# Performance work log

Hardware: AMD Instinct MI355X
Metric: run time of the kernel (lower is better)

The kernel has to match this reference:

```python
import jax, jax.numpy as jnp
import numpy as np

NEG_INF = -1e30


def setup_inputs() -> dict:
    B, S, H, N, T = 128, 512, 512, 256, 40960
    key = jax.random.key(0)
    ks = jax.random.split(key, 20)
    sc = 1.0 / np.sqrt(H)
    inp = {
        'tok_feat': jax.random.normal(ks[0], (B, S, H), jnp.float32),
        'ast_h': jax.random.normal(ks[1], (T, H), jnp.float32),
        'cfg_feat': jax.random.normal(ks[2], (B, N, H), jnp.float32),
        'W_tok': jax.random.normal(ks[3], (H, H), jnp.float32) * sc,
        'b_tok': jax.random.normal(ks[4], (H,), jnp.float32) * 0.01,
        'v_tok': jax.random.normal(ks[5], (H,), jnp.float32) * sc,
        'c_tok': jnp.float32(0.0),
        'W_ast': jax.random.normal(ks[6], (H, H), jnp.float32) * sc,
        'b_ast': jax.random.normal(ks[7], (H,), jnp.float32) * 0.01,
        'v_ast': jax.random.normal(ks[8], (H,), jnp.float32) * sc,
        'c_ast': jnp.float32(0.0),
        'W_cfg': jax.random.normal(ks[9], (H, H), jnp.float32) * sc,
        'b_cfg': jax.random.normal(ks[10], (H,), jnp.float32) * 0.01,
        'v_cfg': jax.random.normal(ks[11], (H,), jnp.float32) * sc,
        'c_cfg': jnp.float32(0.0),
        'W_fuse': jax.random.normal(ks[12], (3 * H, H), jnp.float32) * (1.0 / np.sqrt(3 * H)),
        'b_fuse': jax.random.normal(ks[13], (H,), jnp.float32) * 0.01,
        'tok_len': jax.random.randint(ks[14], (B,), 1, S + 1, jnp.int64),
        # ragged AST: sorted segment ids covering T nodes, here equal-size segments
        'node_seg': jnp.repeat(jnp.arange(B, dtype=jnp.int32), T // B),
        'cfg_node_mask': jax.random.randint(ks[15], (B, N), 0, 2, jnp.int32).at[:, 0].set(1),
    }
    return inp


def reference(tok_feat, ast_h, cfg_feat,
              W_tok, b_tok, v_tok, c_tok,
              W_ast, b_ast, v_ast, c_ast,
              W_cfg, b_cfg, v_cfg, c_cfg,
              W_fuse, b_fuse,
              tok_len, node_seg, cfg_node_mask):
    B, S, H = tok_feat.shape
    N = cfg_feat.shape[1]

    # ---- Token modality: masked softmax attention pooling ----
    tok_logit = jnp.tanh(tok_feat @ W_tok + b_tok) @ v_tok + c_tok          # [B,S]
    tok_mask = jnp.arange(S)[None, :] < tok_len[:, None]                    # [B,S]
    tok_w = jax.nn.softmax(jnp.where(tok_mask, tok_logit, NEG_INF), axis=1)
    tok_pool = jnp.einsum('bs,bsh->bh', tok_w, tok_feat)                    # [B,H]

    # ---- AST modality: ragged segment softmax attention pooling ----
    ast_logit = jnp.tanh(ast_h @ W_ast + b_ast) @ v_ast + c_ast             # [T]
    seg_max = jax.ops.segment_max(ast_logit, node_seg, num_segments=B)
    e = jnp.exp(ast_logit - seg_max[node_seg])
    denom = jax.ops.segment_sum(e, node_seg, num_segments=B)
    ast_w = e / denom[node_seg]                                             # [T]
    ast_pool = jax.ops.segment_sum(ast_w[:, None] * ast_h, node_seg, num_segments=B)  # [B,H]

    # ---- CFG modality: masked sigmoid-gated pooling ----
    cfg_logit = jnp.tanh(cfg_feat @ W_cfg + b_cfg) @ v_cfg + c_cfg          # [B,N]
    gate = jax.nn.sigmoid(cfg_logit) * cfg_node_mask.astype(cfg_feat.dtype)
    cfg_pool = jnp.einsum('bn,bnh->bh', gate, cfg_feat)                     # [B,H]

    # ---- Modal fusion ----
    concat = jnp.concatenate([tok_pool, ast_pool, cfg_pool], axis=1)        # [B,3H]
    code_feat = jnp.tanh(concat @ W_fuse + b_fuse)                          # [B,H]
    return code_feat
```

## Files before the change

### kernel.cpp

```cpp
#include <hip/hip_runtime.h>
#include <stdint.h>

#define HD 512

typedef __bf16 bf16x8 __attribute__((ext_vector_type(8)));
typedef __bf16 bf16x4 __attribute__((ext_vector_type(4)));
typedef float  f32x4  __attribute__((ext_vector_type(4)));

union BF8U { uint4 u; bf16x8 v; };

__device__ __forceinline__ float fast_tanh(float x) {
  x = fminf(15.f, fmaxf(-15.f, x));
  float e = __expf(2.f * x);
  return (e - 1.f) * __builtin_amdgcn_rcpf(e + 1.f);
}
__device__ __forceinline__ float fast_sigmoid(float x) {
  return __builtin_amdgcn_rcpf(1.f + __expf(-x));
}

__global__ void setup_kernel(const float* __restrict__ W0, const float* __restrict__ W1,
                             const float* __restrict__ W2, unsigned short* __restrict__ WbAll,
                             float4* __restrict__ zdst, int nz,
                             const int* __restrict__ seg, int* __restrict__ ss,
                             int* __restrict__ se, int T) {
  int blk = blockIdx.x, t = threadIdx.x;
  if (blk < 192) {
    int mat = blk >> 6, chunk = blk & 63;
    const float* W = (mat == 0) ? W0 : ((mat == 1) ? W1 : W2);
    int np = chunk >> 4, kt = chunk & 15;
    int jl = t & 127, kh = t >> 7;
    int j = np * 128 + jl;
    int nt = jl >> 4;
    unsigned short* base = WbAll + (size_t)mat * 262144 + (size_t)chunk * 4096 + nt * 512;
#pragma unroll
    for (int i = 0; i < 16; ++i) {
      int kk = kh * 16 + i;
      float v = W[(size_t)(kt * 32 + kk) * HD + j];
      int l = (kk >> 3) * 16 + (jl & 15);
      int jj = kk & 7;
      union { __bf16 h; unsigned short u; } cv;
      cv.h = (__bf16)v;
      base[l * 8 + jj] = cv.u;
    }
  } else if (blk < 384) {
    int i = (blk - 192) * 256 + t;
    if (i < nz) zdst[i] = make_float4(0.f, 0.f, 0.f, 0.f);
  } else {
    int tt = (blk - 384) * 256 + t;
    if (tt < T) {
      int s = seg[tt];
      if (tt == 0 || seg[tt - 1] != s) ss[s] = tt;
      if (tt == T - 1 || seg[tt + 1] != s) se[s] = tt + 1;
    }
  }
}

__global__ __launch_bounds__(512, 4) void gemm_all_kernel(
    const float* __restrict__ A0, const float* __restrict__ A1, const float* __restrict__ A2,
    const unsigned short* __restrict__ WbAll,
    const float* __restrict__ b0, const float* __restrict__ v0,
    const float* __restrict__ b1, const float* __restrict__ v1,
    const float* __restrict__ b2, const float* __restrict__ v2,
    const int* __restrict__ tokLen, int nTok, int nAst,
    float* __restrict__ lg0, float* __restrict__ lg1, float* __restrict__ lg2)
{
  int bm = blockIdx.x;
  const float* A; const unsigned short* Wb; const float* bias; const float* vvec;
  float* logit; int lb;
  if (bm < nTok) {
    lb = bm; A = A0; Wb = WbAll; bias = b0; vvec = v0; logit = lg0;
    bool i64 = (tokLen[1] == 0);
    int b = lb >> 3;
    int len = i64 ? tokLen[2 * b] : tokLen[b];
    if (((lb & 7) * 64) >= len) return;
  } else if (bm < nTok + nAst) {
    lb = bm - nTok; A = A1; Wb = WbAll + 262144; bias = b1; vvec = v1; logit = lg1;
  } else {
    lb = bm - nTok - nAst; A = A2; Wb = WbAll + 524288; bias = b2; vvec = v2; logit = lg2;
  }
  size_t m0 = (size_t)lb * 64;

  int tid = threadIdx.x, wave = tid >> 6, lane = tid & 63;
  int wn = wave;

  __shared__ __align__(16) char AshB[2][4096];
  __shared__ float redS[8][64];

  const float* aSrc = A + (m0 + (tid >> 3)) * HD + (tid & 7) * 4;
  const int rowS = tid >> 3, qS = tid & 7;
  const int srW = rowS >> 1;
  const int wA = srW * 128 + 16 * ((((rowS & 1) << 2) + (qS >> 1)) ^ (srW & 7)) + (qS & 1) * 8;

  const char* srcB = (const char*)Wb + (size_t)(wn >> 1) * 131072 +
                     (wn & 1) * 4096 + lane * 16;

  const int aRd = ((lane & 15) >> 1) * 128 +
                  16 * ((4 * (lane & 1) + (lane >> 4)) ^ ((lane & 15) >> 1));

  float4 a4;
  auto loadA = [&](float4& dst, int kt) {
    dst = *(const float4*)(aSrc + kt * 32);
  };
  auto writeA = [&](int buf, const float4& ar) {
    bf16x4 w0;
    w0[0] = (__bf16)ar.x; w0[1] = (__bf16)ar.y; w0[2] = (__bf16)ar.z; w0[3] = (__bf16)ar.w;
    *(bf16x4*)(&AshB[buf][0] + wA) = w0;
  };
  auto loadB = [&](bf16x8 (&dst)[4], int kt) {
    const char* sB = srcB + (size_t)kt * 8192;
#pragma unroll
    for (int ntl = 0; ntl < 4; ++ntl) {
      BF8U bu;
      bu.u = *(const uint4*)(sB + ntl * 1024);
      dst[ntl] = bu.v;
    }
  };

  f32x4 acc[4][4];
#pragma unroll
  for (int i = 0; i < 4; ++i)
#pragma unroll
    for (int j = 0; j < 4; ++j) acc[i][j] = (f32x4){0.f, 0.f, 0.f, 0.f};

  bf16x8 bfA[4], bfB[4];

  {
    float4 t4;
    loadA(t4, 0);
    writeA(0, t4);
    loadA(a4, 1);
    loadB(bfA, 0);
    asm volatile("s_waitcnt lgkmcnt(0)" ::: "memory");
    __builtin_amdgcn_s_barrier();
  }

  auto body = [&](int kt, bf16x8 (&cur)[4], bf16x8 (&nxt)[4]) {
    if (kt < 15) loadB(nxt, kt + 1);
    const char* aBuf = &AshB[kt & 1][0];
    {
      bf16x8 af2[2];
      af2[0] = *(const bf16x8*)(aBuf + 0 * 1024 + aRd);
      af2[1] = *(const bf16x8*)(aBuf + 1 * 1024 + aRd);
#pragma unroll
      for (int mt = 0; mt < 2; ++mt)
#pragma unroll
        for (int ntl = 0; ntl < 4; ++ntl)
          acc[mt][ntl] = __builtin_amdgcn_mfma_f32_16x16x32_bf16(af2[mt], cur[ntl], acc[mt][ntl], 0, 0, 0);
    }
    {
      bf16x8 af2[2];
      af2[0] = *(const bf16x8*)(aBuf + 2 * 1024 + aRd);
      af2[1] = *(const bf16x8*)(aBuf + 3 * 1024 + aRd);
#pragma unroll
      for (int mt = 0; mt < 2; ++mt)
#pragma unroll
        for (int ntl = 0; ntl < 4; ++ntl)
          acc[2 + mt][ntl] = __builtin_amdgcn_mfma_f32_16x16x32_bf16(af2[mt], cur[ntl], acc[2 + mt][ntl], 0, 0, 0);
    }
    if (kt < 15) {
      writeA((kt + 1) & 1, a4);
      if (kt < 14) loadA(a4, kt + 2);
      asm volatile("s_waitcnt lgkmcnt(0)" ::: "memory");
      __builtin_amdgcn_s_barrier();
    }
  };

#pragma unroll
  for (int kt = 0; kt < 16; kt += 2) {
    body(kt, bfA, bfB);
    body(kt + 1, bfB, bfA);
  }

  float part[4][4];
#pragma unroll
  for (int mt = 0; mt < 4; ++mt)
#pragma unroll
    for (int i = 0; i < 4; ++i) part[mt][i] = 0.f;

  const int colBase = wn * 64;
#pragma unroll
  for (int ntl = 0; ntl < 4; ++ntl) {
    int j = colBase + ntl * 16 + (lane & 15);
    float bj = bias[j], vj = vvec[j];
#pragma unroll
    for (int mt = 0; mt < 4; ++mt)
#pragma unroll
      for (int i = 0; i < 4; ++i)
        part[mt][i] += fast_tanh(acc[mt][ntl][i] + bj) * vj;
  }
#pragma unroll
  for (int off = 8; off >= 1; off >>= 1)
#pragma unroll
    for (int mt = 0; mt < 4; ++mt)
#pragma unroll
      for (int i = 0; i < 4; ++i)
        part[mt][i] += __shfl_xor(part[mt][i], off, 64);

  if ((lane & 15) == 0) {
    int rloc = (lane >> 4) * 4;
#pragma unroll
    for (int mt = 0; mt < 4; ++mt)
#pragma unroll
      for (int i = 0; i < 4; ++i)
        redS[wn][mt * 16 + rloc + i] = part[mt][i];
  }
  __syncthreads();
  if (tid < 64) {
    float s = 0.f;
#pragma unroll
    for (int w = 0; w < 8; ++w) s += redS[w][tid];
    logit[m0 + tid] = s;
  }
}

__global__ void pool_all_kernel(
    const float* __restrict__ tokf, const float* __restrict__ lgT, const int* __restrict__ tl,
    const float* __restrict__ astf, const float* __restrict__ lgA,
    const int* __restrict__ ss, const int* __restrict__ se,
    const float* __restrict__ cfgf, const float* __restrict__ lgC,
    const int* __restrict__ mask, const float* __restrict__ cptr,
    float* __restrict__ pools)
{
  int b = blockIdx.x, chz = blockIdx.y, tid = threadIdx.x;
  __shared__ float redm[4], reds[4];
  __shared__ float wsh[128];
  int wv = tid >> 6, ln = tid & 63;

  if (chz < 4) {
    int ch = chz;
    bool i64 = (tl[1] == 0);
    int len = i64 ? tl[2 * b] : tl[b];
    if (ch * 128 >= len) return;
    const float* lg = lgT + b * 512;
    float x0 = (tid < len) ? lg[tid] : -1e30f;
    float x1 = (tid + 256 < len) ? lg[tid + 256] : -1e30f;
    float m = fmaxf(x0, x1);
#pragma unroll
    for (int off = 32; off; off >>= 1) m = fmaxf(m, __shfl_xor(m, off, 64));
    if (ln == 0) redm[wv] = m;
    __syncthreads();
    float bm = fmaxf(fmaxf(redm[0], redm[1]), fmaxf(redm[2], redm[3]));
    float s = ((tid < len) ? __expf(x0 - bm) : 0.f) + ((tid + 256 < len) ? __expf(x1 - bm) : 0.f);
#pragma unroll
    for (int off = 32; off; off >>= 1) s += __shfl_xor(s, off, 64);
    if (ln == 0) reds[wv] = s;
    __syncthreads();
    float bs = reds[0] + reds[1] + reds[2] + reds[3];
    float rb = __builtin_amdgcn_rcpf(bs);
    if (tid < 128) {
      int sidx = ch * 128 + tid;
      wsh[tid] = (sidx < len) ? __expf(lg[sidx] - bm) * rb : 0.f;
    }
    __syncthreads();
    int cnt = min(128, len - ch * 128);
    int h = tid * 2;
    float2 acc = make_float2(0.f, 0.f);
    const float* fb = tokf + ((size_t)b * 512 + ch * 128) * HD + h;
#pragma unroll 4
    for (int s2 = 0; s2 < cnt; ++s2) {
      float2 f = *(const float2*)(fb + (size_t)s2 * HD);
      acc.x += wsh[s2] * f.x; acc.y += wsh[s2] * f.y;
    }
    atomicAdd(&pools[b * 512 + h], acc.x);
    atomicAdd(&pools[b * 512 + h + 1], acc.y);
  } else if (chz < 8) {
    int ch = chz - 4;
    int t0 = ss[b], t1 = se[b];
    int len = t1 - t0;
    if (len <= 0) return;
    float m = -1e30f;
    for (int t = t0 + tid; t < t1; t += 256) m = fmaxf(m, lgA[t]);
#pragma unroll
    for (int off = 32; off; off >>= 1) m = fmaxf(m, __shfl_xor(m, off, 64));
    if (ln == 0) redm[wv] = m;
    __syncthreads();
    float bm = fmaxf(fmaxf(redm[0], redm[1]), fmaxf(redm[2], redm[3]));
    float s = 0.f;
    for (int t = t0 + tid; t < t1; t += 256) s += __expf(lgA[t] - bm);
#pragma unroll
    for (int off = 32; off; off >>= 1) s += __shfl_xor(s, off, 64);
    if (ln == 0) reds[wv] = s;
    __syncthreads();
    float bs = reds[0] + reds[1] + reds[2] + reds[3];
    float r = __builtin_amdgcn_rcpf(bs);
    int per = (len + 3) >> 2;
    int a0 = t0 + ch * per;
    int a1 = min(t1, a0 + per);
    int h = tid * 2;
    float2 acc = make_float2(0.f, 0.f);
    for (int base = a0; base < a1; base += 128) {
      int cnt = min(128, a1 - base);
      __syncthreads();
      if (tid < cnt) wsh[tid] = __expf(lgA[base + tid] - bm) * r;
      __syncthreads();
      for (int s2 = 0; s2 < cnt; ++s2) {
        float2 f = *(const float2*)(astf + (size_t)(base + s2) * HD + h);
        acc.x += wsh[s2] * f.x; acc.y += wsh[s2] * f.y;
      }
    }
    atomicAdd(&pools[65536 + b * 512 + h], acc.x);
    atomicAdd(&pools[65536 + b * 512 + h + 1], acc.y);
  } else {
    int ch = chz - 8;
    float cc = cptr[0];
    int n0 = ch * 128;
    if (tid < 128) {
      int n = n0 + tid;
      float g = fast_sigmoid(lgC[b * 256 + n] + cc);
      wsh[tid] = mask[b * 256 + n] ? g : 0.f;
    }
    __syncthreads();
    int h = tid * 2;
    float2 acc = make_float2(0.f, 0.f);
    const float* fb = cfgf + ((size_t)b * 256 + n0) * HD + h;
#pragma unroll 4
    for (int s2 = 0; s2 < 128; ++s2) {
      float2 f = *(const float2*)(fb + (size_t)s2 * HD);
      acc.x += wsh[s2] * f.x; acc.y += wsh[s2] * f.y;
    }
    atomicAdd(&pools[131072 + b * 512 + h], acc.x);
    atomicAdd(&pools[131072 + b * 512 + h + 1], acc.y);
  }
}

__global__ void fuse_partial_kernel(const float* __restrict__ pools,
                                    const float* __restrict__ Wf,
                                    float* __restrict__ fpart) {
  int bg = blockIdx.x, kc = blockIdx.y;
  int tid = threadIdx.x;
  int bq = tid >> 7, jt = tid & 127;
  __shared__ float psh[8][128];
  for (int idx = tid; idx < 8 * 128; idx += 256) {
    int bb = idx >> 7, kk = idx & 127;
    int i = kc * 128 + kk;
    psh[bb][kk] = pools[(size_t)(i >> 9) * 65536 + (size_t)(bg * 8 + bb) * 512 + (i & 511)];
  }
  __syncthreads();
  f32x4 acc[4];
#pragma unroll
  for (int bb = 0; bb < 4; ++bb) acc[bb] = (f32x4){0.f, 0.f, 0.f, 0.f};
  const float* wrow = Wf + (size_t)(kc * 128) * 512 + jt * 4;
#pragma unroll 4
  for (int k = 0; k < 128; ++k) {
    float4 wv = *(const float4*)(wrow + (size_t)k * 512);
#pragma unroll
    for (int bb = 0; bb < 4; ++bb) {
      float p = psh[bq * 4 + bb][k];
      acc[bb][0] += p * wv.x; acc[bb][1] += p * wv.y;
      acc[bb][2] += p * wv.z; acc[bb][3] += p * wv.w;
    }
  }
  float* dst = fpart + (size_t)kc * 65536 + (size_t)(bg * 8 + bq * 4) * 512 + jt * 4;
#pragma unroll
  for (int bb = 0; bb < 4; ++bb)
    *(f32x4*)(dst + (size_t)bb * 512) = acc[bb];
}

__global__ void finalize_kernel(const float* __restrict__ fpart, const float* __restrict__ bfuse,
                                float* __restrict__ out) {
  int idx = blockIdx.x * 256 + threadIdx.x;
  float s = bfuse[idx & 511];
#pragma unroll
  for (int kc = 0; kc < 12; ++kc) s += fpart[(size_t)kc * 65536 + idx];
  out[idx] = fast_tanh(s);
}

static constexpr size_t OFF_WB_ALL = 0;
static constexpr size_t OFF_LG_TOK = 1536 * 1024;
static constexpr size_t OFF_LG_AST = OFF_LG_TOK + 65536 * 4;
static constexpr size_t OFF_LG_CFG = OFF_LG_AST + 40960 * 4;
static constexpr size_t OFF_POOLS  = OFF_LG_CFG + 32768 * 4;
static constexpr size_t OFF_SS     = OFF_POOLS + 3 * 65536 * 4;
static constexpr size_t OFF_SE     = OFF_SS + 512;
static constexpr size_t OFF_FPART  = OFF_SE + 512;
static constexpr int    ZERO_N4    = (3 * 65536 * 4) / 16;

extern "C" void kernel_launch(void* const* d_in, const int* in_sizes, int n_in,
                              void* d_out, int out_size, void* d_ws, size_t ws_size,
                              hipStream_t stream) {
  const float* tok_feat = (const float*)d_in[0];
  const float* ast_h    = (const float*)d_in[1];
  const float* cfg_feat = (const float*)d_in[2];
  const float* W_tok = (const float*)d_in[3];
  const float* b_tok = (const float*)d_in[4];
  const float* v_tok = (const float*)d_in[5];
  const float* W_ast = (const float*)d_in[7];
  const float* b_ast = (const float*)d_in[8];
  const float* v_ast = (const float*)d_in[9];
  const float* W_cfg = (const float*)d_in[11];
  const float* b_cfg = (const float*)d_in[12];
  const float* v_cfg = (const float*)d_in[13];
  const float* c_cfg = (const float*)d_in[14];
  const float* W_fuse = (const float*)d_in[15];
  const float* b_fuse = (const float*)d_in[16];
  const int* tok_len  = (const int*)d_in[17];
  const int* node_seg = (const int*)d_in[18];
  const int* cfg_mask = (const int*)d_in[19];

  const int M_tok = in_sizes[0] / HD;
  const int T_ast = in_sizes[1] / HD;
  const int M_cfg = in_sizes[2] / HD;
  const int nTok = M_tok / 64, nAst = T_ast / 64, nCfg = M_cfg / 64;

  char* ws = (char*)d_ws;
  unsigned short* wbAll = (unsigned short*)(ws + OFF_WB_ALL);
  float* lgTok = (float*)(ws + OFF_LG_TOK);
  float* lgAst = (float*)(ws + OFF_LG_AST);
  float* lgCfg = (float*)(ws + OFF_LG_CFG);
  float* pools = (float*)(ws + OFF_POOLS);
  int*   ss    = (int*)(ws + OFF_SS);
  int*   se    = (int*)(ws + OFF_SE);
  float* fpart = (float*)(ws + OFF_FPART);

  int segBlks = (T_ast + 255) / 256;
  setup_kernel<<<384 + segBlks, 256, 0, stream>>>(
      W_tok, W_ast, W_cfg, wbAll, (float4*)(ws + OFF_POOLS), ZERO_N4,
      node_seg, ss, se, T_ast);

  gemm_all_kernel<<<nTok + nAst + nCfg, 512, 0, stream>>>(
      tok_feat, ast_h, cfg_feat, wbAll,
      b_tok, v_tok, b_ast, v_ast, b_cfg, v_cfg,
      tok_len, nTok, nAst, lgTok, lgAst, lgCfg);

  pool_all_kernel<<<dim3(128, 10), 256, 0, stream>>>(
      tok_feat, lgTok, tok_len,
      ast_h, lgAst, ss, se,
      cfg_feat, lgCfg, cfg_mask, c_cfg, pools);

  fuse_partial_kernel<<<dim3(16, 12), 256, 0, stream>>>(pools, W_fuse, fpart);
  finalize_kernel<<<256, 256, 0, stream>>>(fpart, b_fuse, (float*)d_out);
}
```

Measured before the change: 158.1 us.

## Retile logit GEMM to 128-row blocks split across two column halves with atomics

Each GEMM workgroup now covers 128 rows and half of the 512 output columns, so each wave handles 32 columns across 8 M-tiles instead of 64 columns across 4. The two column halves combine their partial logits with atomicAdd, which means the logit buffers must be zeroed, so the setup kernel's zeroing range is extended to cover them. A loads are widened to 8 floats per thread. The aim is to get more reuse of each B fragment from registers and fewer B global loads per MFMA, at the cost of atomics, extra zeroing, and coarser 128-row skipping of masked token rows.

```diff
diff --git a/kernel.cpp b/kernel.cpp
--- a/kernel.cpp
+++ b/kernel.cpp
@@ -4,7 +4,6 @@
 #define HD 512
 
 typedef __bf16 bf16x8 __attribute__((ext_vector_type(8)));
-typedef __bf16 bf16x4 __attribute__((ext_vector_type(4)));
 typedef float  f32x4  __attribute__((ext_vector_type(4)));
 
 union BF8U { uint4 u; bf16x8 v; };
@@ -42,11 +41,11 @@
       cv.h = (__bf16)v;
       base[l * 8 + jj] = cv.u;
     }
-  } else if (blk < 384) {
+  } else if (blk < 576) {
     int i = (blk - 192) * 256 + t;
     if (i < nz) zdst[i] = make_float4(0.f, 0.f, 0.f, 0.f);
   } else {
-    int tt = (blk - 384) * 256 + t;
+    int tt = (blk - 576) * 256 + t;
     if (tt < T) {
       int s = seg[tt];
       if (tt == 0 || seg[tt - 1] != s) ss[s] = tt;
@@ -72,60 +71,62 @@
     bool i64 = (tokLen[1] == 0);
     int b = lb >> 3;
     int len = i64 ? tokLen[2 * b] : tokLen[b];
-    if (((lb & 7) * 64) >= len) return;
+    if ((((lb >> 1) & 3) * 128) >= len) return;
   } else if (bm < nTok + nAst) {
     lb = bm - nTok; A = A1; Wb = WbAll + 262144; bias = b1; vvec = v1; logit = lg1;
   } else {
     lb = bm - nTok - nAst; A = A2; Wb = WbAll + 524288; bias = b2; vvec = v2; logit = lg2;
   }
-  size_t m0 = (size_t)lb * 64;
+  int r = lb >> 1, c = lb & 1;
+  size_t m0 = (size_t)r * 128;
 
   int tid = threadIdx.x, wave = tid >> 6, lane = tid & 63;
   int wn = wave;
 
-  __shared__ __align__(16) char AshB[2][4096];
-  __shared__ float redS[8][64];
-
-  const float* aSrc = A + (m0 + (tid >> 3)) * HD + (tid & 7) * 4;
-  const int rowS = tid >> 3, qS = tid & 7;
+  __shared__ __align__(16) char AshB[2][8192];
+  __shared__ float redS[8][128];
+
+  const float* aSrc = A + (m0 + (tid >> 2)) * HD + (tid & 3) * 8;
+  const int rowS = tid >> 2, qS = tid & 3;
   const int srW = rowS >> 1;
-  const int wA = srW * 128 + 16 * ((((rowS & 1) << 2) + (qS >> 1)) ^ (srW & 7)) + (qS & 1) * 8;
-
-  const char* srcB = (const char*)Wb + (size_t)(wn >> 1) * 131072 +
-                     (wn & 1) * 4096 + lane * 16;
+  const int wA = srW * 128 + 16 * ((((rowS & 1) << 2) + qS) ^ (srW & 7));
+
+  const char* srcB = (const char*)Wb + (size_t)(c * 2 + (wn >> 2)) * 131072 +
+                     ((wn & 3) * 2) * 1024 + lane * 16;
 
   const int aRd = ((lane & 15) >> 1) * 128 +
                   16 * ((4 * (lane & 1) + (lane >> 4)) ^ ((lane & 15) >> 1));
 
-  float4 a4;
-  auto loadA = [&](float4& dst, int kt) {
-    dst = *(const float4*)(aSrc + kt * 32);
+  float4 a4[2];
+  auto loadA = [&](float4 (&dst)[2], int kt) {
+    const float* p = aSrc + kt * 32;
+    dst[0] = *(const float4*)(p);
+    dst[1] = *(const float4*)(p + 4);
   };
-  auto writeA = [&](int buf, const float4& ar) {
-    bf16x4 w0;
-    w0[0] = (__bf16)ar.x; w0[1] = (__bf16)ar.y; w0[2] = (__bf16)ar.z; w0[3] = (__bf16)ar.w;
-    *(bf16x4*)(&AshB[buf][0] + wA) = w0;
+  auto writeA = [&](int buf, const float4 (&ar)[2]) {
+    bf16x8 w0;
+    w0[0] = (__bf16)ar[0].x; w0[1] = (__bf16)ar[0].y; w0[2] = (__bf16)ar[0].z; w0[3] = (__bf16)ar[0].w;
+    w0[4] = (__bf16)ar[1].x; w0[5] = (__bf16)ar[1].y; w0[6] = (__bf16)ar[1].z; w0[7] = (__bf16)ar[1].w;
+    *(bf16x8*)(&AshB[buf][0] + wA) = w0;
   };
-  auto loadB = [&](bf16x8 (&dst)[4], int kt) {
+  auto loadB = [&](bf16x8 (&dst)[2], int kt) {
     const char* sB = srcB + (size_t)kt * 8192;
-#pragma unroll
-    for (int ntl = 0; ntl < 4; ++ntl) {
-      BF8U bu;
-      bu.u = *(const uint4*)(sB + ntl * 1024);
-      dst[ntl] = bu.v;
-    }
+    BF8U bu0, bu1;
+    bu0.u = *(const uint4*)(sB);
+    bu1.u = *(const uint4*)(sB + 1024);
+    dst[0] = bu0.v; dst[1] = bu1.v;
   };
 
-  f32x4 acc[4][4];
-#pragma unroll
-  for (int i = 0; i < 4; ++i)
-#pragma unroll
-    for (int j = 0; j < 4; ++j) acc[i][j] = (f32x4){0.f, 0.f, 0.f, 0.f};
-
-  bf16x8 bfA[4], bfB[4];
+  f32x4 acc[8][2];
+#pragma unroll
+  for (int i = 0; i < 8; ++i)
+#pragma unroll
+    for (int j = 0; j < 2; ++j) acc[i][j] = (f32x4){0.f, 0.f, 0.f, 0.f};
+
+  bf16x8 bfA[2], bfB[2];
 
   {
-    float4 t4;
+    float4 t4[2];
     loadA(t4, 0);
     writeA(0, t4);
     loadA(a4, 1);
@@ -134,28 +135,20 @@
     __builtin_amdgcn_s_barrier();
   }
 
-  auto body = [&](int kt, bf16x8 (&cur)[4], bf16x8 (&nxt)[4]) {
+  auto body = [&](int kt, bf16x8 (&cur)[2], bf16x8 (&nxt)[2]) {
     if (kt < 15) loadB(nxt, kt + 1);
     const char* aBuf = &AshB[kt & 1][0];
-    {
+#pragma unroll
+    for (int mg = 0; mg < 4; ++mg) {
       bf16x8 af2[2];
-      af2[0] = *(const bf16x8*)(aBuf + 0 * 1024 + aRd);
-      af2[1] = *(const bf16x8*)(aBuf + 1 * 1024 + aRd);
-#pragma unroll
-      for (int mt = 0; mt < 2; ++mt)
-#pragma unroll
-        for (int ntl = 0; ntl < 4; ++ntl)
-          acc[mt][ntl] = __builtin_amdgcn_mfma_f32_16x16x32_bf16(af2[mt], cur[ntl], acc[mt][ntl], 0, 0, 0);
-    }
-    {
-      bf16x8 af2[2];
-      af2[0] = *(const bf16x8*)(aBuf + 2 * 1024 + aRd);
-      af2[1] = *(const bf16x8*)(aBuf + 3 * 1024 + aRd);
-#pragma unroll
-      for (int mt = 0; mt < 2; ++mt)
-#pragma unroll
-        for (int ntl = 0; ntl < 4; ++ntl)
-          acc[2 + mt][ntl] = __builtin_amdgcn_mfma_f32_16x16x32_bf16(af2[mt], cur[ntl], acc[2 + mt][ntl], 0, 0, 0);
+      af2[0] = *(const bf16x8*)(aBuf + (mg * 2 + 0) * 1024 + aRd);
+      af2[1] = *(const bf16x8*)(aBuf + (mg * 2 + 1) * 1024 + aRd);
+#pragma unroll
+      for (int m2 = 0; m2 < 2; ++m2)
+#pragma unroll
+        for (int ntl = 0; ntl < 2; ++ntl)
+          acc[mg * 2 + m2][ntl] =
+              __builtin_amdgcn_mfma_f32_16x16x32_bf16(af2[m2], cur[ntl], acc[mg * 2 + m2][ntl], 0, 0, 0);
     }
     if (kt < 15) {
       writeA((kt + 1) & 1, a4);
@@ -171,19 +164,19 @@
     body(kt + 1, bfB, bfA);
   }
 
-  float part[4][4];
-#pragma unroll
-  for (int mt = 0; mt < 4; ++mt)
+  float part[8][4];
+#pragma unroll
+  for (int mt = 0; mt < 8; ++mt)
 #pragma unroll
     for (int i = 0; i < 4; ++i) part[mt][i] = 0.f;
 
-  const int colBase = wn * 64;
-#pragma unroll
-  for (int ntl = 0; ntl < 4; ++ntl) {
+  const int colBase = c * 256 + wn * 32;
+#pragma unroll
+  for (int ntl = 0; ntl < 2; ++ntl) {
     int j = colBase + ntl * 16 + (lane & 15);
     float bj = bias[j], vj = vvec[j];
 #pragma unroll
-    for (int mt = 0; mt < 4; ++mt)
+    for (int mt = 0; mt < 8; ++mt)
 #pragma unroll
       for (int i = 0; i < 4; ++i)
         part[mt][i] += fast_tanh(acc[mt][ntl][i] + bj) * vj;
@@ -191,7 +184,7 @@
 #pragma unroll
   for (int off = 8; off >= 1; off >>= 1)
 #pragma unroll
-    for (int mt = 0; mt < 4; ++mt)
+    for (int mt = 0; mt < 8; ++mt)
 #pragma unroll
       for (int i = 0; i < 4; ++i)
         part[mt][i] += __shfl_xor(part[mt][i], off, 64);
@@ -199,17 +192,17 @@
   if ((lane & 15) == 0) {
     int rloc = (lane >> 4) * 4;
 #pragma unroll
-    for (int mt = 0; mt < 4; ++mt)
+    for (int mt = 0; mt < 8; ++mt)
 #pragma unroll
       for (int i = 0; i < 4; ++i)
         redS[wn][mt * 16 + rloc + i] = part[mt][i];
   }
   __syncthreads();
-  if (tid < 64) {
+  if (tid < 128) {
     float s = 0.f;
 #pragma unroll
     for (int w = 0; w < 8; ++w) s += redS[w][tid];
-    logit[m0 + tid] = s;
+    atomicAdd(&logit[m0 + tid], s);
   }
 }
 
@@ -373,7 +366,7 @@
 static constexpr size_t OFF_SS     = OFF_POOLS + 3 * 65536 * 4;
 static constexpr size_t OFF_SE     = OFF_SS + 512;
 static constexpr size_t OFF_FPART  = OFF_SE + 512;
-static constexpr int    ZERO_N4    = (3 * 65536 * 4) / 16;
+static constexpr int    ZERO_N4    = (int)(((139264 + 3 * 65536) * 4) / 16);
 
 extern "C" void kernel_launch(void* const* d_in, const int* in_sizes, int n_in,
                               void* d_out, int out_size, void* d_ws, size_t ws_size,
@@ -413,8 +406,8 @@
   float* fpart = (float*)(ws + OFF_FPART);
 
   int segBlks = (T_ast + 255) / 256;
-  setup_kernel<<<384 + segBlks, 256, 0, stream>>>(
-      W_tok, W_ast, W_cfg, wbAll, (float4*)(ws + OFF_POOLS), ZERO_N4,
+  setup_kernel<<<576 + segBlks, 256, 0, stream>>>(
+      W_tok, W_ast, W_cfg, wbAll, (float4*)(ws + OFF_LG_TOK), ZERO_N4,
       node_seg, ss, se, T_ast);
 
   gemm_all_kernel<<<nTok + nAst + nCfg, 512, 0, stream>>>(
```

Result: slower. 176.3 us (+11.5%).
